# Kernel optimization log

Hardware: AMD Instinct MI355X
Metric: run time of the kernel (lower is better)

The kernel has to match this reference:

```python
import jax, jax.numpy as jnp
import numpy as np

L, D, H, B, T = 16, 256, 128, 32, 2048  # labels, input_dim, hidden (D//2), batch, seq_len


def setup_inputs() -> dict:
    key = jax.random.key(0)
    ks = jax.random.split(key, 6)
    inputs = jax.random.normal(ks[0], (B, T, D), dtype=jnp.float32)
    # variable lengths in [T//2, T], mask = 1 for valid positions
    lengths = jax.random.randint(ks[1], (B,), T // 2, T + 1)
    attention_mask = (jnp.arange(T)[None, :] < lengths[:, None]).astype(jnp.int32)
    s = 1.0 / np.sqrt(H)  # PyTorch GRU init range
    Wih = jax.random.uniform(ks[2], (L, 2, 3 * H, D), jnp.float32, -s, s)
    Whh = jax.random.uniform(ks[3], (L, 2, 3 * H, H), jnp.float32, -s, s)
    bih = jax.random.uniform(ks[4], (L, 2, 3 * H), jnp.float32, -s, s)
    bhh = jax.random.uniform(ks[5], (L, 2, 3 * H), jnp.float32, -s, s)
    label = jnp.arange(L, dtype=jnp.int64)
    return {"inputs": inputs, "attention_mask": attention_mask, "label": label,
            "Wih": Wih, "Whh": Whh, "bih": bih, "bhh": bhh}


def _gru_sweep(xs, mask, Wih, Whh, bih, bhh, reverse):
    """Run L independent GRUs over time with per-step validity masking.
    xs: [T,B,D], mask: [T,B] bool, Wih: [L,3H,D], Whh: [L,3H,H], bih/bhh: [L,3H].
    Returns final hidden [L,B,H]. Masked (padded) steps leave h unchanged, which
    for reverse=True reproduces packed-sequence backward-direction semantics
    (h0 carried untouched until t = len-1, then updated down to t = 0)."""
    h0 = jnp.zeros((Wih.shape[0], xs.shape[1], Whh.shape[-1]), xs.dtype)

    def step(h, inp):
        x_t, m_t = inp  # [B,D], [B]
        gi = jnp.einsum('bd,lgd->lbg', x_t, Wih) + bih[:, None, :]   # [L,B,3H]
        gh = jnp.einsum('lbh,lgh->lbg', h, Whh) + bhh[:, None, :]    # [L,B,3H]
        ir, iz, i_n = jnp.split(gi, 3, axis=-1)
        hr, hz, h_n = jnp.split(gh, 3, axis=-1)
        r = jax.nn.sigmoid(ir + hr)
        z = jax.nn.sigmoid(iz + hz)
        n = jnp.tanh(i_n + r * h_n)
        h_new = (1.0 - z) * n + z * h
        h = jnp.where(m_t[None, :, None], h_new, h)
        return h, None

    h_fin, _ = jax.lax.scan(step, h0, (xs, mask), reverse=reverse)
    return h_fin


def reference(inputs, attention_mask, label, Wih, Whh, bih, bhh):
    # select the GRUs for the given labels (train path iterates `label`)
    Wih_l, Whh_l = Wih[label], Whh[label]            # [L,2,3H,D], [L,2,3H,H]
    bih_l, bhh_l = bih[label], bhh[label]            # [L,2,3H]
    xs = jnp.transpose(inputs, (1, 0, 2))            # [T,B,D]
    mask = attention_mask.astype(bool).T             # [T,B]
    h_fwd = _gru_sweep(xs, mask, Wih_l[:, 0], Whh_l[:, 0], bih_l[:, 0], bhh_l[:, 0], reverse=False)
    h_bwd = _gru_sweep(xs, mask, Wih_l[:, 1], Whh_l[:, 1], bih_l[:, 1], bhh_l[:, 1], reverse=True)
    # torch.cat([h_n[-1], h_n[-2]]) = [backward_final, forward_final]
    out = jnp.concatenate([h_bwd, h_fwd], axis=-1)   # [L,B,2H]
    return jnp.transpose(out, (1, 0, 2))             # [B,L,2H] == [B,L,D]
```

## Files before the change

kernel.cpp:

```cpp
#include <hip/hip_runtime.h>


typedef unsigned short u16;
typedef unsigned int   u32;
using bf16x8 = __attribute__((ext_vector_type(8))) short;
using f32x4  = __attribute__((ext_vector_type(4))) float;

#define BLKW    1536
#define TSTRIDE 393216

#define KS_RZ (-1.4426950408889634f)
#define KS_N  (-2.8853900817779268f)

__device__ __forceinline__ u16 f2b(float f) {
  union { float f; u32 u; } v; v.f = f;
  u32 r = (v.u + 0x7fffu + ((v.u >> 16) & 1u)) >> 16;
  return (u16)r;
}
__device__ __forceinline__ u32 pack_bf16(float a, float b) {
#if __has_builtin(__builtin_amdgcn_cvt_pk_bf16_f32)
  auto pk = __builtin_amdgcn_cvt_pk_bf16_f32(a, b);
  union { decltype(pk) v; u32 u; } cv; cv.v = pk;
  return cv.u;
#else
  return (u32)f2b(a) | ((u32)f2b(b) << 16);
#endif
}
__device__ __forceinline__ float blo(u32 u) {
  union { u32 u; float f; } v; v.u = u << 16; return v.f;
}
__device__ __forceinline__ float bhi(u32 u) {
  union { u32 u; float f; } v; v.u = u & 0xffff0000u; return v.f;
}
__device__ __forceinline__ void lds16(u16* l, const u16* g) {
  __builtin_amdgcn_global_load_lds(
      (const __attribute__((address_space(1))) void*)g,
      (__attribute__((address_space(3))) void*)(unsigned long long)l,
      16, 0, 0);
}
__device__ __forceinline__ float sig2(float xs) {
  return __builtin_amdgcn_rcpf(1.f + __builtin_amdgcn_exp2f(xs));
}
__device__ __forceinline__ void softbarrier() {
  __builtin_amdgcn_sched_barrier(0);
  __builtin_amdgcn_s_waitcnt(0xC07F);
  __builtin_amdgcn_s_barrier();
  __builtin_amdgcn_sched_barrier(0);
}

__global__ void cvt_wih(const float* __restrict__ in, u16* __restrict__ o, int n) {
  int i = (blockIdx.x * 256 + threadIdx.x) * 4;
  if (i >= n) return;
  float s = (((i >> 15) % 3) == 2) ? KS_N : KS_RZ;
  float4 v = *(const float4*)(in + i);
  uint2 u; u.x = pack_bf16(v.x * s, v.y * s); u.y = pack_bf16(v.z * s, v.w * s);
  *(uint2*)(o + i) = u;
}
__global__ void cvt_whh(const float* __restrict__ in, u16* __restrict__ o, int n) {
  int i = (blockIdx.x * 256 + threadIdx.x) * 4;
  if (i >= n) return;
  float s = (((i >> 14) % 3) == 2) ? KS_N : KS_RZ;
  float4 v = *(const float4*)(in + i);
  uint2 u; u.x = pack_bf16(v.x * s, v.y * s); u.y = pack_bf16(v.z * s, v.w * s);
  *(uint2*)(o + i) = u;
}
__global__ void xpose(const float* __restrict__ x, u16* __restrict__ X) {
  int idx = blockIdx.x * 256 + threadIdx.x;
  int kc = idx & 63, tb = idx >> 6;
  int b = tb & 31, t = tb >> 5;
  float4 v = *(const float4*)(x + ((size_t)(b * 2048 + t) * 256 + kc * 4));
  uint2 u; u.x = pack_bf16(v.x, v.y); u.y = pack_bf16(v.z, v.w);
  *(uint2*)(X + ((size_t)tb * 256 + kc * 4)) = u;
}

__global__ __launch_bounds__(512, 1) void combo(
    const u16* __restrict__ X, const u16* __restrict__ Wib,
    const float* __restrict__ bih, const float* __restrict__ bhh,
    char* __restrict__ gw_f, char* __restrict__ gw_b, int tw_f, int tw_b, int n_gemm,
    const char* __restrict__ gr_f, const char* __restrict__ gr_b, int tr_f, int tr_b,
    const u16* __restrict__ Whb, const int* __restrict__ mask,
    float* __restrict__ hst, float* __restrict__ out,
    int Tc, int n_rec, int first, int last) {
  __shared__ __align__(16) char smem[49152];
  const int tid = threadIdx.x, lane = tid & 63;
  const int a = lane & 15, q = lane >> 4;

  if ((int)blockIdx.x >= n_rec) {
    const int g = blockIdx.x - n_rec;
    if (g >= n_gemm) return;
    const int mtiles = Tc >> 2;
    const int pair = g % 24;
    const int rest = g / 24;
    const int mb = rest % mtiles;
    const int dg = rest / mtiles;
    const int tbase = dg ? tw_b : tw_f;
    char* gi = dg ? gw_b : gw_f;

    const int w8 = tid >> 6, half = w8 >> 2, w4 = w8 & 3;
    const int mw = (w4 >> 1) * 64, nw = (w4 & 1) * 64;
    const int nti = pair * 2 + half;
    const int lidx = nti / 3, g3 = nti % 3, g0 = g3 * 128;

    u16* As = (u16*)smem;
    u16* Bs = (u16*)(smem + 16384 + half * 16384);
    const u16* Ag = X + (size_t)(tbase * 32 + mb * 128) * 256;
    const u16* Bg = Wib + (size_t)((lidx * 2 + dg) * 384 + g0) * 256;

    f32x4 acc[4][4];
    for (int i = 0; i < 4; ++i)
      for (int jj = 0; jj < 4; ++jj) acc[i][jj] = f32x4{0.f, 0.f, 0.f, 0.f};

    const int r8 = lane >> 3, kc = lane & 7;
    for (int kt = 0; kt < 4; ++kt) {
      for (int i = 0; i < 2; ++i) {
        int slot = w8 * 2 + i, row = slot * 8 + r8;
        lds16(&As[slot * 512 + lane * 8], Ag + (size_t)row * 256 + kt * 64 + kc * 8);
      }
      for (int i = 0; i < 4; ++i) {
        int slot = w4 * 4 + i, row = slot * 8 + r8;
        lds16(&Bs[slot * 512 + lane * 8], Bg + (size_t)row * 256 + kt * 64 + kc * 8);
      }
      __syncthreads();
      for (int ks = 0; ks < 2; ++ks) {
        bf16x8 Af[4], Bf[4];
        for (int mt = 0; mt < 4; ++mt)
          Af[mt] = *(const bf16x8*)&As[(mw + mt * 16 + a) * 64 + ks * 32 + q * 8];
        for (int nt = 0; nt < 4; ++nt)
          Bf[nt] = *(const bf16x8*)&Bs[(nw + nt * 16 + a) * 64 + ks * 32 + q * 8];
        for (int mt = 0; mt < 4; ++mt)
          for (int nt = 0; nt < 4; ++nt)
            acc[mt][nt] = __builtin_amdgcn_mfma_f32_16x16x32_bf16(
                Af[mt], Bf[nt], acc[mt][nt], 0, 0, 0);
      }
      __syncthreads();
    }
    for (int nt = 0; nt < 4; ++nt) {
      int gg = g0 + nw + nt * 16 + a;
      int gidx = (lidx * 2 + dg) * 384 + gg;
      float bias = (g3 == 2) ? KS_N * bih[gidx]
                             : KS_RZ * (bih[gidx] + bhh[gidx]);
      int wj = (nw + nt * 16) >> 4;
      for (int mt = 0; mt < 4; ++mt) {
        int rowbase = mb * 128 + mw + mt * 16;
        int t_loc = rowbase >> 5;
        int bh = (rowbase >> 4) & 1;
        uint2 uv;
        uv.x = pack_bf16(acc[mt][nt][0] + bias, acc[mt][nt][1] + bias);
        uv.y = pack_bf16(acc[mt][nt][2] + bias, acc[mt][nt][3] + bias);
        *(uint2*)(gi + (size_t)t_loc * TSTRIDE +
                  (size_t)((lidx * 2 + bh) * 8 + wj) * BLKW + g3 * 512 +
                  (q * 16 + a) * 8) = uv;
      }
    }
    return;
  }

  const int bid = blockIdx.x;
  const int bh = bid & 1, d = (bid >> 1) & 1, l = bid >> 2;
  const int w = tid >> 6;
  const int bbase = bh * 16;
  const int j = w * 16 + a;
  const int wofs = (l * 2 + d) * 384;

  u16* hb = (u16*)smem;
  int* lenS = (int*)(smem + 8704);

  bf16x8 Bf[3][4];
  for (int g3 = 0; g3 < 3; ++g3)
    for (int kf = 0; kf < 4; ++kf)
      Bf[g3][kf] = *(const bf16x8*)(Whb + (size_t)(wofs + g3 * 128 + j) * 128 + kf * 32 + q * 8);
  float bn = KS_N * bhh[wofs + 2 * 128 + j];
  f32x4 bc4 = f32x4{bn, bn, bn, bn};

  for (int rr = w; rr < 16; rr += 8) {
    int s = 0;
    const int* mp = mask + (size_t)(bbase + rr) * 2048;
    for (int t = lane; t < 2048; t += 64) s += mp[t];
    for (int off = 32; off; off >>= 1) s += __shfl_down(s, off);
    if (lane == 0) lenS[rr] = s;
  }

  float h[4];
  if (first) { h[0] = h[1] = h[2] = h[3] = 0.f; }
  else {
    for (int r = 0; r < 4; ++r)
      h[r] = hst[(size_t)((l * 2 + d) * 32 + bbase + q * 4 + r) * 128 + j];
  }
  {
    u32 k01 = pack_bf16(h[0], h[1]), k23 = pack_bf16(h[2], h[3]);
    u16* dst = &hb[(q * 4) * 136 + j];
    dst[0] = (u16)k01; dst[136] = (u16)(k01 >> 16);
    dst[272] = (u16)k23; dst[408] = (u16)(k23 >> 16);
  }
  __syncthreads();

  int len[4], mx = 0;
  for (int r = 0; r < 4; ++r) len[r] = lenS[q * 4 + r];
  for (int rr = 0; rr < 16; ++rr) mx = max(mx, lenS[rr]);

  const char* gi = d ? gr_b : gr_f;
  const int tb = d ? tr_b : tr_f;
  const size_t cbase = (size_t)((l * 2 + bh) * 8 + w) * BLKW + (q * 16 + a) * 8;

  int tl_lo, tl_hi;
  if (d == 0) { tl_lo = 0;
    int te = mx - tb;
    tl_hi = te <= 0 ? 0 : (te >= Tc ? Tc : ((te + 3) & ~3));
  } else { tl_hi = Tc;
    int ts = tb + Tc - mx;
    tl_lo = ts <= 0 ? 0 : (ts >= Tc ? Tc : (ts & ~3));
  }

  int p = 0;
  uint2 P[4][3];
  auto issue = [&](uint2 (&Pb)[3], int tl) {
    int tll = tl < Tc ? tl : Tc - 1;
    int t2 = d ? (Tc - 1 - tll) : tll;
    const char* bp = gi + (size_t)t2 * TSTRIDE + cbase;
    Pb[0] = *(const uint2*)(bp);
    Pb[1] = *(const uint2*)(bp + 512);
    Pb[2] = *(const uint2*)(bp + 1024);
  };
  issue(P[0], tl_lo); issue(P[1], tl_lo + 1);
  issue(P[2], tl_lo + 2); issue(P[3], tl_lo + 3);

  auto step = [&](int tl, uint2 (&Pb)[3]) {
    f32x4 Cr = f32x4{blo(Pb[0].x), bhi(Pb[0].x), blo(Pb[0].y), bhi(Pb[0].y)};
    f32x4 Cz = f32x4{blo(Pb[1].x), bhi(Pb[1].x), blo(Pb[1].y), bhi(Pb[1].y)};
    float nf[4] = { blo(Pb[2].x), bhi(Pb[2].x), blo(Pb[2].y), bhi(Pb[2].y) };
    issue(Pb, tl + 4);
    int t_loc = d ? (Tc - 1 - tl) : tl;
    int t_glob = tb + t_loc;

    bf16x8 Af[4];
    for (int kf = 0; kf < 4; ++kf)
      Af[kf] = *(const bf16x8*)&hb[p * 2176 + a * 136 + kf * 32 + q * 8];
    f32x4 a0 = __builtin_amdgcn_mfma_f32_16x16x32_bf16(Af[0], Bf[0][0], Cr, 0, 0, 0);
    f32x4 a1 = __builtin_amdgcn_mfma_f32_16x16x32_bf16(Af[0], Bf[1][0], Cz, 0, 0, 0);
    f32x4 a2 = __builtin_amdgcn_mfma_f32_16x16x32_bf16(Af[0], Bf[2][0], bc4, 0, 0, 0);
    for (int kf = 1; kf < 4; ++kf) {
      a0 = __builtin_amdgcn_mfma_f32_16x16x32_bf16(Af[kf], Bf[0][kf], a0, 0, 0, 0);
      a1 = __builtin_amdgcn_mfma_f32_16x16x32_bf16(Af[kf], Bf[1][kf], a1, 0, 0, 0);
      a2 = __builtin_amdgcn_mfma_f32_16x16x32_bf16(Af[kf], Bf[2][kf], a2, 0, 0, 0);
    }
    for (int r = 0; r < 4; ++r) {
      float rg = sig2(a0[r]);
      float zg = sig2(a1[r]);
      float ng = fmaf(2.f, sig2(fmaf(rg, a2[r], nf[r])), -1.f);
      float hv = fmaf(zg, h[r] - ng, ng);
      h[r] = (t_glob < len[r]) ? hv : h[r];
    }
    u32 k01 = pack_bf16(h[0], h[1]), k23 = pack_bf16(h[2], h[3]);
    u16* dst = &hb[(p ^ 1) * 2176 + (q * 4) * 136 + j];
    dst[0] = (u16)k01; dst[136] = (u16)(k01 >> 16);
    dst[272] = (u16)k23; dst[408] = (u16)(k23 >> 16);
    softbarrier();
    p ^= 1;
  };

  for (int tl = tl_lo; tl < tl_hi; tl += 4) {
    step(tl, P[0]);
    step(tl + 1, P[1]);
    step(tl + 2, P[2]);
    step(tl + 3, P[3]);
  }

  if (last) {
    for (int r = 0; r < 4; ++r)
      out[(size_t)((bbase + q * 4 + r) * 16 + l) * 256 + (d ? j : 128 + j)] = h[r];
  } else {
    for (int r = 0; r < 4; ++r)
      hst[(size_t)((l * 2 + d) * 32 + bbase + q * 4 + r) * 128 + j] = h[r];
  }
}

extern "C" void kernel_launch(void* const* d_in, const int* in_sizes, int n_in,
                              void* d_out, int out_size, void* d_ws, size_t ws_size,
                              hipStream_t stream) {
  const float* x    = (const float*)d_in[0];
  const int*   mask = (const int*)d_in[1];
  const float* Wih  = (const float*)d_in[3];
  const float* Whh  = (const float*)d_in[4];
  const float* bih  = (const float*)d_in[5];
  const float* bhh  = (const float*)d_in[6];
  float* out = (float*)d_out;

  char* ws = (char*)d_ws;
  size_t off = 0;
  auto alloc = [&](size_t bytes) -> void* {
    void* p = ws + off; off += (bytes + 255) & ~(size_t)255; return p;
  };
  u16*  Wib = (u16*)alloc(3145728ull * 2);
  u16*  Whb = (u16*)alloc(1572864ull * 2);
  u16*  X   = (u16*)alloc(16777216ull * 2);
  float* hst = (float*)alloc(131072ull * 4);
  size_t fixed = off;

  int Tc = 2048;
  while (Tc > 8 && fixed + 4ull * Tc * TSTRIDE > ws_size) Tc >>= 1;
  char* gi[2][2];
  for (int pp = 0; pp < 2; ++pp)
    for (int dd = 0; dd < 2; ++dd)
      gi[pp][dd] = (char*)alloc((size_t)Tc * TSTRIDE);
  int Nc = 2048 / Tc;
  int NG = 24 * (Tc / 4) * 2;

  cvt_wih<<<3145728 / 4 / 256, 256, 0, stream>>>(Wih, Wib, 3145728);
  cvt_whh<<<1572864 / 4 / 256, 256, 0, stream>>>(Whh, Whb, 1572864);
  xpose<<<16384, 256, 0, stream>>>(x, X);

  combo<<<NG, 512, 0, stream>>>(X, Wib, bih, bhh,
                                gi[0][0], gi[0][1], 0, (Nc - 1) * Tc, NG,
                                gi[0][0], gi[0][1], 0, 0,
                                Whb, mask, hst, out, Tc, 0, 0, 0);

  for (int c = 0; c < Nc; ++c) {
    int par = c & 1, parn = par ^ 1;
    int hasg = (c + 1 < Nc);
    int ng = hasg ? NG : 0;
    combo<<<64 + ng, 512, 0, stream>>>(X, Wib, bih, bhh,
        gi[parn][0], gi[parn][1], (c + 1) * Tc, (Nc - 2 - c) * Tc, ng,
        gi[par][0], gi[par][1], c * Tc, (Nc - 1 - c) * Tc,
        Whb, mask, hst, out, Tc, 64, c == 0, c == Nc - 1);
  }
}
```

Baseline: 1.506 ms.

## Split recurrent blocks to 8 batch rows each, doubling recurrence block count

Each recurrent block now owns 8 batch rows instead of 16, so 128 recurrent blocks run instead of 64 and each thread carries 2 hidden values instead of 4. The precomputed input-gate buffer is relaid out to a 768-byte per-warp stride with 4-byte per-lane loads to match. Launch bounds move to 2 blocks per CU. The MFMA still computes 16 rows with half of them padding, so the per-step latency chain stays about the same while the elementwise work per thread halves. The intent is to spread the serial recurrence across more CUs and shorten each step, at the cost of wasted MFMA rows and twice the Whh register loads across blocks.

```diff
diff --git a/kernel.cpp b/kernel.cpp
--- a/kernel.cpp
+++ b/kernel.cpp
@@ -6,8 +6,8 @@
 using bf16x8 = __attribute__((ext_vector_type(8))) short;
 using f32x4  = __attribute__((ext_vector_type(4))) float;
 
-#define BLKW    1536
 #define TSTRIDE 393216
+#define BLKW    768
 
 #define KS_RZ (-1.4426950408889634f)
 #define KS_N  (-2.8853900817779268f)
@@ -73,7 +73,7 @@
   *(uint2*)(X + ((size_t)tb * 256 + kc * 4)) = u;
 }
 
-__global__ __launch_bounds__(512, 1) void combo(
+__global__ __launch_bounds__(512, 2) void combo(
     const u16* __restrict__ X, const u16* __restrict__ Wib,
     const float* __restrict__ bih, const float* __restrict__ bhh,
     char* __restrict__ gw_f, char* __restrict__ gw_b, int tw_f, int tw_b, int n_gemm,
@@ -139,26 +139,28 @@
       int gidx = (lidx * 2 + dg) * 384 + gg;
       float bias = (g3 == 2) ? KS_N * bih[gidx]
                              : KS_RZ * (bih[gidx] + bhh[gidx]);
-      int wj = (nw + nt * 16) >> 4;
+      int wj = ((nw + nt * 16) >> 4);
       for (int mt = 0; mt < 4; ++mt) {
         int rowbase = mb * 128 + mw + mt * 16;
         int t_loc = rowbase >> 5;
-        int bh = (rowbase >> 4) & 1;
-        uint2 uv;
-        uv.x = pack_bf16(acc[mt][nt][0] + bias, acc[mt][nt][1] + bias);
-        uv.y = pack_bf16(acc[mt][nt][2] + bias, acc[mt][nt][3] + bias);
-        *(uint2*)(gi + (size_t)t_loc * TSTRIDE +
-                  (size_t)((lidx * 2 + bh) * 8 + wj) * BLKW + g3 * 512 +
-                  (q * 16 + a) * 8) = uv;
+        int b0 = (rowbase & 31) + q * 4;
+        int bq0 = b0 >> 3, q0 = (b0 >> 1) & 3;
+        int bq1 = (b0 + 2) >> 3, q1 = ((b0 + 2) >> 1) & 3;
+        char* p0 = gi + (size_t)t_loc * TSTRIDE +
+                   (size_t)((lidx * 4 + bq0) * 8 + wj) * BLKW + g3 * 256 + (q0 * 16 + a) * 4;
+        char* p1 = gi + (size_t)t_loc * TSTRIDE +
+                   (size_t)((lidx * 4 + bq1) * 8 + wj) * BLKW + g3 * 256 + (q1 * 16 + a) * 4;
+        *(u32*)p0 = pack_bf16(acc[mt][nt][0] + bias, acc[mt][nt][1] + bias);
+        *(u32*)p1 = pack_bf16(acc[mt][nt][2] + bias, acc[mt][nt][3] + bias);
       }
     }
     return;
   }
 
   const int bid = blockIdx.x;
-  const int bh = bid & 1, d = (bid >> 1) & 1, l = bid >> 2;
+  const int bq = bid & 3, d = (bid >> 2) & 1, l = bid >> 3;
   const int w = tid >> 6;
-  const int bbase = bh * 16;
+  const int bbase = bq * 8;
   const int j = w * 16 + a;
   const int wofs = (l * 2 + d) * 384;
 
@@ -172,35 +174,34 @@
   float bn = KS_N * bhh[wofs + 2 * 128 + j];
   f32x4 bc4 = f32x4{bn, bn, bn, bn};
 
-  for (int rr = w; rr < 16; rr += 8) {
+  if (w < 8) {
     int s = 0;
-    const int* mp = mask + (size_t)(bbase + rr) * 2048;
+    const int* mp = mask + (size_t)(bbase + w) * 2048;
     for (int t = lane; t < 2048; t += 64) s += mp[t];
     for (int off = 32; off; off >>= 1) s += __shfl_down(s, off);
-    if (lane == 0) lenS[rr] = s;
-  }
-
-  float h[4];
-  if (first) { h[0] = h[1] = h[2] = h[3] = 0.f; }
+    if (lane == 0) lenS[w] = s;
+  }
+
+  float h0, h1;
+  if (first) { h0 = h1 = 0.f; }
   else {
-    for (int r = 0; r < 4; ++r)
-      h[r] = hst[(size_t)((l * 2 + d) * 32 + bbase + q * 4 + r) * 128 + j];
+    h0 = hst[(size_t)((l * 2 + d) * 32 + bbase + q * 2 + 0) * 128 + j];
+    h1 = hst[(size_t)((l * 2 + d) * 32 + bbase + q * 2 + 1) * 128 + j];
   }
   {
-    u32 k01 = pack_bf16(h[0], h[1]), k23 = pack_bf16(h[2], h[3]);
+    u32 k = pack_bf16(h0, h1);
     u16* dst = &hb[(q * 4) * 136 + j];
-    dst[0] = (u16)k01; dst[136] = (u16)(k01 >> 16);
-    dst[272] = (u16)k23; dst[408] = (u16)(k23 >> 16);
+    dst[0] = (u16)k; dst[136] = (u16)(k >> 16);
   }
   __syncthreads();
 
-  int len[4], mx = 0;
-  for (int r = 0; r < 4; ++r) len[r] = lenS[q * 4 + r];
-  for (int rr = 0; rr < 16; ++rr) mx = max(mx, lenS[rr]);
+  int len0 = lenS[q * 2 + 0], len1 = lenS[q * 2 + 1];
+  int mx = 0;
+  for (int rr = 0; rr < 8; ++rr) mx = max(mx, lenS[rr]);
 
   const char* gi = d ? gr_b : gr_f;
   const int tb = d ? tr_b : tr_f;
-  const size_t cbase = (size_t)((l * 2 + bh) * 8 + w) * BLKW + (q * 16 + a) * 8;
+  const char* gbase = gi + (size_t)((l * 4 + bq) * 8 + w) * BLKW + lane * 4;
 
   int tl_lo, tl_hi;
   if (d == 0) { tl_lo = 0;
@@ -212,22 +213,22 @@
   }
 
   int p = 0;
-  uint2 P[4][3];
-  auto issue = [&](uint2 (&Pb)[3], int tl) {
+  uint3 P[4];
+  auto issue = [&](uint3& Pb, int tl) {
     int tll = tl < Tc ? tl : Tc - 1;
     int t2 = d ? (Tc - 1 - tll) : tll;
-    const char* bp = gi + (size_t)t2 * TSTRIDE + cbase;
-    Pb[0] = *(const uint2*)(bp);
-    Pb[1] = *(const uint2*)(bp + 512);
-    Pb[2] = *(const uint2*)(bp + 1024);
+    const char* bp = gbase + (size_t)t2 * TSTRIDE;
+    Pb.x = *(const u32*)(bp);
+    Pb.y = *(const u32*)(bp + 256);
+    Pb.z = *(const u32*)(bp + 512);
   };
   issue(P[0], tl_lo); issue(P[1], tl_lo + 1);
   issue(P[2], tl_lo + 2); issue(P[3], tl_lo + 3);
 
-  auto step = [&](int tl, uint2 (&Pb)[3]) {
-    f32x4 Cr = f32x4{blo(Pb[0].x), bhi(Pb[0].x), blo(Pb[0].y), bhi(Pb[0].y)};
-    f32x4 Cz = f32x4{blo(Pb[1].x), bhi(Pb[1].x), blo(Pb[1].y), bhi(Pb[1].y)};
-    float nf[4] = { blo(Pb[2].x), bhi(Pb[2].x), blo(Pb[2].y), bhi(Pb[2].y) };
+  auto step = [&](int tl, uint3& Pb) {
+    f32x4 Cr = f32x4{blo(Pb.x), bhi(Pb.x), 0.f, 0.f};
+    f32x4 Cz = f32x4{blo(Pb.y), bhi(Pb.y), 0.f, 0.f};
+    float nf0 = blo(Pb.z), nf1 = bhi(Pb.z);
     issue(Pb, tl + 4);
     int t_loc = d ? (Tc - 1 - tl) : tl;
     int t_glob = tb + t_loc;
@@ -243,17 +244,23 @@
       a1 = __builtin_amdgcn_mfma_f32_16x16x32_bf16(Af[kf], Bf[1][kf], a1, 0, 0, 0);
       a2 = __builtin_amdgcn_mfma_f32_16x16x32_bf16(Af[kf], Bf[2][kf], a2, 0, 0, 0);
     }
-    for (int r = 0; r < 4; ++r) {
-      float rg = sig2(a0[r]);
-      float zg = sig2(a1[r]);
-      float ng = fmaf(2.f, sig2(fmaf(rg, a2[r], nf[r])), -1.f);
-      float hv = fmaf(zg, h[r] - ng, ng);
-      h[r] = (t_glob < len[r]) ? hv : h[r];
-    }
-    u32 k01 = pack_bf16(h[0], h[1]), k23 = pack_bf16(h[2], h[3]);
+    {
+      float rg = sig2(a0[0]);
+      float zg = sig2(a1[0]);
+      float ng = fmaf(2.f, sig2(fmaf(rg, a2[0], nf0)), -1.f);
+      float hv = fmaf(zg, h0 - ng, ng);
+      h0 = (t_glob < len0) ? hv : h0;
+    }
+    {
+      float rg = sig2(a0[1]);
+      float zg = sig2(a1[1]);
+      float ng = fmaf(2.f, sig2(fmaf(rg, a2[1], nf1)), -1.f);
+      float hv = fmaf(zg, h1 - ng, ng);
+      h1 = (t_glob < len1) ? hv : h1;
+    }
+    u32 k = pack_bf16(h0, h1);
     u16* dst = &hb[(p ^ 1) * 2176 + (q * 4) * 136 + j];
-    dst[0] = (u16)k01; dst[136] = (u16)(k01 >> 16);
-    dst[272] = (u16)k23; dst[408] = (u16)(k23 >> 16);
+    dst[0] = (u16)k; dst[136] = (u16)(k >> 16);
     softbarrier();
     p ^= 1;
   };
@@ -266,11 +273,11 @@
   }
 
   if (last) {
-    for (int r = 0; r < 4; ++r)
-      out[(size_t)((bbase + q * 4 + r) * 16 + l) * 256 + (d ? j : 128 + j)] = h[r];
+    out[(size_t)((bbase + q * 2 + 0) * 16 + l) * 256 + (d ? j : 128 + j)] = h0;
+    out[(size_t)((bbase + q * 2 + 1) * 16 + l) * 256 + (d ? j : 128 + j)] = h1;
   } else {
-    for (int r = 0; r < 4; ++r)
-      hst[(size_t)((l * 2 + d) * 32 + bbase + q * 4 + r) * 128 + j] = h[r];
+    hst[(size_t)((l * 2 + d) * 32 + bbase + q * 2 + 0) * 128 + j] = h0;
+    hst[(size_t)((l * 2 + d) * 32 + bbase + q * 2 + 1) * 128 + j] = h1;
   }
 }
 
@@ -318,9 +325,9 @@
     int par = c & 1, parn = par ^ 1;
     int hasg = (c + 1 < Nc);
     int ng = hasg ? NG : 0;
-    combo<<<64 + ng, 512, 0, stream>>>(X, Wib, bih, bhh,
+    combo<<<128 + ng, 512, 0, stream>>>(X, Wib, bih, bhh,
         gi[parn][0], gi[parn][1], (c + 1) * Tc, (Nc - 2 - c) * Tc, ng,
         gi[par][0], gi[par][1], c * Tc, (Nc - 1 - c) * Tc,
-        Whb, mask, hst, out, Tc, 64, c == 0, c == Nc - 1);
-  }
-}
+        Whb, mask, hst, out, Tc, 128, c == 0, c == Nc - 1);
+  }
+}
```

Result: slower. 1.562 ms (+3.7%).

## Run GRU recurrence on four waves each owning two hidden column tiles

Applied to the files above, without the earlier changes.

The recurrent step is redistributed so only four of the eight waves compute, each handling two 16-column tiles of the hidden state with six MFMA chains instead of three. The gate-precompute layout and the LDS hidden buffer layout change to match, with 16-byte loads of precomputed gates and a new transposed hb indexing. The prefetch depth drops from four steps to two. The other four waves only participate in the soft barriers. This aims to cut per-step synchronisation cost and LDS traffic among fewer waves, at the cost of more serial work per wave and shallower prefetch.

```diff
diff --git a/kernel.cpp b/kernel.cpp
--- a/kernel.cpp
+++ b/kernel.cpp
@@ -6,8 +6,8 @@
 using bf16x8 = __attribute__((ext_vector_type(8))) short;
 using f32x4  = __attribute__((ext_vector_type(4))) float;
 
-#define BLKW    1536
 #define TSTRIDE 393216
+#define BLKW    3072
 
 #define KS_RZ (-1.4426950408889634f)
 #define KS_N  (-2.8853900817779268f)
@@ -135,11 +135,11 @@
       __syncthreads();
     }
     for (int nt = 0; nt < 4; ++nt) {
-      int gg = g0 + nw + nt * 16 + a;
-      int gidx = (lidx * 2 + dg) * 384 + gg;
+      int j = nw + nt * 16 + a;
+      int gidx = (lidx * 2 + dg) * 384 + g0 + j;
       float bias = (g3 == 2) ? KS_N * bih[gidx]
                              : KS_RZ * (bih[gidx] + bhh[gidx]);
-      int wj = (nw + nt * 16) >> 4;
+      int wj = j >> 5, ct = (j >> 4) & 1;
       for (int mt = 0; mt < 4; ++mt) {
         int rowbase = mb * 128 + mw + mt * 16;
         int t_loc = rowbase >> 5;
@@ -148,8 +148,8 @@
         uv.x = pack_bf16(acc[mt][nt][0] + bias, acc[mt][nt][1] + bias);
         uv.y = pack_bf16(acc[mt][nt][2] + bias, acc[mt][nt][3] + bias);
         *(uint2*)(gi + (size_t)t_loc * TSTRIDE +
-                  (size_t)((lidx * 2 + bh) * 8 + wj) * BLKW + g3 * 512 +
-                  (q * 16 + a) * 8) = uv;
+                  (size_t)((lidx * 2 + bh) * 4 + wj) * BLKW + g3 * 1024 +
+                  (q * 16 + a) * 16 + ct * 8) = uv;
       }
     }
     return;
@@ -159,118 +159,153 @@
   const int bh = bid & 1, d = (bid >> 1) & 1, l = bid >> 2;
   const int w = tid >> 6;
   const int bbase = bh * 16;
-  const int j = w * 16 + a;
   const int wofs = (l * 2 + d) * 384;
+  const int jc0 = w * 32 + a, jc1 = jc0 + 16;
 
   u16* hb = (u16*)smem;
-  int* lenS = (int*)(smem + 8704);
-
-  bf16x8 Bf[3][4];
-  for (int g3 = 0; g3 < 3; ++g3)
-    for (int kf = 0; kf < 4; ++kf)
-      Bf[g3][kf] = *(const bf16x8*)(Whb + (size_t)(wofs + g3 * 128 + j) * 128 + kf * 32 + q * 8);
-  float bn = KS_N * bhh[wofs + 2 * 128 + j];
-  f32x4 bc4 = f32x4{bn, bn, bn, bn};
-
-  for (int rr = w; rr < 16; rr += 8) {
+  int* lenS = (int*)(smem + 8192);
+
+  {
     int s = 0;
-    const int* mp = mask + (size_t)(bbase + rr) * 2048;
+    const int* mp = mask + (size_t)(bbase + w) * 2048;
     for (int t = lane; t < 2048; t += 64) s += mp[t];
     for (int off = 32; off; off >>= 1) s += __shfl_down(s, off);
-    if (lane == 0) lenS[rr] = s;
-  }
-
-  float h[4];
-  if (first) { h[0] = h[1] = h[2] = h[3] = 0.f; }
-  else {
-    for (int r = 0; r < 4; ++r)
-      h[r] = hst[(size_t)((l * 2 + d) * 32 + bbase + q * 4 + r) * 128 + j];
-  }
-  {
-    u32 k01 = pack_bf16(h[0], h[1]), k23 = pack_bf16(h[2], h[3]);
-    u16* dst = &hb[(q * 4) * 136 + j];
-    dst[0] = (u16)k01; dst[136] = (u16)(k01 >> 16);
-    dst[272] = (u16)k23; dst[408] = (u16)(k23 >> 16);
+    if (lane == 0) lenS[w] = s;
+    s = 0;
+    mp = mask + (size_t)(bbase + w + 8) * 2048;
+    for (int t = lane; t < 2048; t += 64) s += mp[t];
+    for (int off = 32; off; off >>= 1) s += __shfl_down(s, off);
+    if (lane == 0) lenS[w + 8] = s;
+  }
+
+  float h[2][4];
+  if (w < 4) {
+    for (int ct = 0; ct < 2; ++ct) {
+      int jc = ct ? jc1 : jc0;
+      for (int r = 0; r < 4; ++r)
+        h[ct][r] = first ? 0.f
+            : hst[(size_t)((l * 2 + d) * 32 + bbase + q * 4 + r) * 128 + jc];
+      u32 k01 = pack_bf16(h[ct][0], h[ct][1]);
+      u32 k23 = pack_bf16(h[ct][2], h[ct][3]);
+      u16* dst = &hb[(w * 4 + ct * 2 + (a >> 3)) * 128 + (q * 4) * 8 + (a & 7)];
+      dst[0] = (u16)k01; dst[8] = (u16)(k01 >> 16);
+      dst[16] = (u16)k23; dst[24] = (u16)(k23 >> 16);
+    }
   }
   __syncthreads();
 
-  int len[4], mx = 0;
+  int len[4];
   for (int r = 0; r < 4; ++r) len[r] = lenS[q * 4 + r];
+  int mx = 0;
   for (int rr = 0; rr < 16; ++rr) mx = max(mx, lenS[rr]);
 
   const char* gi = d ? gr_b : gr_f;
   const int tb = d ? tr_b : tr_f;
-  const size_t cbase = (size_t)((l * 2 + bh) * 8 + w) * BLKW + (q * 16 + a) * 8;
 
   int tl_lo, tl_hi;
   if (d == 0) { tl_lo = 0;
     int te = mx - tb;
-    tl_hi = te <= 0 ? 0 : (te >= Tc ? Tc : ((te + 3) & ~3));
+    tl_hi = te <= 0 ? 0 : (te >= Tc ? Tc : ((te + 1) & ~1));
   } else { tl_hi = Tc;
     int ts = tb + Tc - mx;
-    tl_lo = ts <= 0 ? 0 : (ts >= Tc ? Tc : (ts & ~3));
-  }
-
+    tl_lo = ts <= 0 ? 0 : (ts >= Tc ? Tc : (ts & ~1));
+  }
+
+  if (w >= 4) {
+    for (int i = tl_lo; i < tl_hi; ++i) softbarrier();
+    return;
+  }
+
+  bf16x8 Bf[3][2][4];
+  for (int g3 = 0; g3 < 3; ++g3)
+    for (int ct = 0; ct < 2; ++ct)
+      for (int kf = 0; kf < 4; ++kf)
+        Bf[g3][ct][kf] = *(const bf16x8*)(
+            Whb + (size_t)(wofs + g3 * 128 + (ct ? jc1 : jc0)) * 128 + kf * 32 + q * 8);
+  float bn0 = KS_N * bhh[wofs + 256 + jc0];
+  float bn1 = KS_N * bhh[wofs + 256 + jc1];
+  f32x4 bc0 = f32x4{bn0, bn0, bn0, bn0};
+  f32x4 bc1 = f32x4{bn1, bn1, bn1, bn1};
+
+  const char* gbase = gi + (size_t)(((l * 2 + bh) * 4 + w)) * BLKW + lane * 16;
+
+  struct GI { uint4 r, z, n; };
   int p = 0;
-  uint2 P[4][3];
-  auto issue = [&](uint2 (&Pb)[3], int tl) {
+  GI P[2];
+  auto issue = [&](GI& Pb, int tl) {
     int tll = tl < Tc ? tl : Tc - 1;
     int t2 = d ? (Tc - 1 - tll) : tll;
-    const char* bp = gi + (size_t)t2 * TSTRIDE + cbase;
-    Pb[0] = *(const uint2*)(bp);
-    Pb[1] = *(const uint2*)(bp + 512);
-    Pb[2] = *(const uint2*)(bp + 1024);
+    const char* bp = gbase + (size_t)t2 * TSTRIDE;
+    Pb.r = *(const uint4*)(bp);
+    Pb.z = *(const uint4*)(bp + 1024);
+    Pb.n = *(const uint4*)(bp + 2048);
   };
   issue(P[0], tl_lo); issue(P[1], tl_lo + 1);
-  issue(P[2], tl_lo + 2); issue(P[3], tl_lo + 3);
-
-  auto step = [&](int tl, uint2 (&Pb)[3]) {
-    f32x4 Cr = f32x4{blo(Pb[0].x), bhi(Pb[0].x), blo(Pb[0].y), bhi(Pb[0].y)};
-    f32x4 Cz = f32x4{blo(Pb[1].x), bhi(Pb[1].x), blo(Pb[1].y), bhi(Pb[1].y)};
-    float nf[4] = { blo(Pb[2].x), bhi(Pb[2].x), blo(Pb[2].y), bhi(Pb[2].y) };
-    issue(Pb, tl + 4);
-    int t_loc = d ? (Tc - 1 - tl) : tl;
-    int t_glob = tb + t_loc;
+
+  auto step = [&](int tl, GI& Pb) {
+    f32x4 Cr0 = f32x4{blo(Pb.r.x), bhi(Pb.r.x), blo(Pb.r.y), bhi(Pb.r.y)};
+    f32x4 Cr1 = f32x4{blo(Pb.r.z), bhi(Pb.r.z), blo(Pb.r.w), bhi(Pb.r.w)};
+    f32x4 Cz0 = f32x4{blo(Pb.z.x), bhi(Pb.z.x), blo(Pb.z.y), bhi(Pb.z.y)};
+    f32x4 Cz1 = f32x4{blo(Pb.z.z), bhi(Pb.z.z), blo(Pb.z.w), bhi(Pb.z.w)};
+    float nf0[4] = { blo(Pb.n.x), bhi(Pb.n.x), blo(Pb.n.y), bhi(Pb.n.y) };
+    float nf1[4] = { blo(Pb.n.z), bhi(Pb.n.z), blo(Pb.n.w), bhi(Pb.n.w) };
+    issue(Pb, tl + 2);
+    int t_glob = tb + (d ? (Tc - 1 - tl) : tl);
 
     bf16x8 Af[4];
     for (int kf = 0; kf < 4; ++kf)
-      Af[kf] = *(const bf16x8*)&hb[p * 2176 + a * 136 + kf * 32 + q * 8];
-    f32x4 a0 = __builtin_amdgcn_mfma_f32_16x16x32_bf16(Af[0], Bf[0][0], Cr, 0, 0, 0);
-    f32x4 a1 = __builtin_amdgcn_mfma_f32_16x16x32_bf16(Af[0], Bf[1][0], Cz, 0, 0, 0);
-    f32x4 a2 = __builtin_amdgcn_mfma_f32_16x16x32_bf16(Af[0], Bf[2][0], bc4, 0, 0, 0);
-    for (int kf = 1; kf < 4; ++kf) {
-      a0 = __builtin_amdgcn_mfma_f32_16x16x32_bf16(Af[kf], Bf[0][kf], a0, 0, 0, 0);
-      a1 = __builtin_amdgcn_mfma_f32_16x16x32_bf16(Af[kf], Bf[1][kf], a1, 0, 0, 0);
-      a2 = __builtin_amdgcn_mfma_f32_16x16x32_bf16(Af[kf], Bf[2][kf], a2, 0, 0, 0);
+      Af[kf] = *(const bf16x8*)&hb[p * 2048 + (kf * 4 + q) * 128 + a * 8];
+    f32x4 r0 = Cr0, r1 = Cr1, z0 = Cz0, z1 = Cz1, n0 = bc0, n1 = bc1;
+    for (int kf = 0; kf < 4; ++kf) {
+      r0 = __builtin_amdgcn_mfma_f32_16x16x32_bf16(Af[kf], Bf[0][0][kf], r0, 0, 0, 0);
+      r1 = __builtin_amdgcn_mfma_f32_16x16x32_bf16(Af[kf], Bf[0][1][kf], r1, 0, 0, 0);
+      z0 = __builtin_amdgcn_mfma_f32_16x16x32_bf16(Af[kf], Bf[1][0][kf], z0, 0, 0, 0);
+      z1 = __builtin_amdgcn_mfma_f32_16x16x32_bf16(Af[kf], Bf[1][1][kf], z1, 0, 0, 0);
+      n0 = __builtin_amdgcn_mfma_f32_16x16x32_bf16(Af[kf], Bf[2][0][kf], n0, 0, 0, 0);
+      n1 = __builtin_amdgcn_mfma_f32_16x16x32_bf16(Af[kf], Bf[2][1][kf], n1, 0, 0, 0);
     }
     for (int r = 0; r < 4; ++r) {
-      float rg = sig2(a0[r]);
-      float zg = sig2(a1[r]);
-      float ng = fmaf(2.f, sig2(fmaf(rg, a2[r], nf[r])), -1.f);
-      float hv = fmaf(zg, h[r] - ng, ng);
-      h[r] = (t_glob < len[r]) ? hv : h[r];
-    }
-    u32 k01 = pack_bf16(h[0], h[1]), k23 = pack_bf16(h[2], h[3]);
-    u16* dst = &hb[(p ^ 1) * 2176 + (q * 4) * 136 + j];
-    dst[0] = (u16)k01; dst[136] = (u16)(k01 >> 16);
-    dst[272] = (u16)k23; dst[408] = (u16)(k23 >> 16);
+      {
+        float rg = sig2(r0[r]);
+        float zg = sig2(z0[r]);
+        float ng = fmaf(2.f, sig2(fmaf(rg, n0[r], nf0[r])), -1.f);
+        float hv = fmaf(zg, h[0][r] - ng, ng);
+        h[0][r] = (t_glob < len[r]) ? hv : h[0][r];
+      }
+      {
+        float rg = sig2(r1[r]);
+        float zg = sig2(z1[r]);
+        float ng = fmaf(2.f, sig2(fmaf(rg, n1[r], nf1[r])), -1.f);
+        float hv = fmaf(zg, h[1][r] - ng, ng);
+        h[1][r] = (t_glob < len[r]) ? hv : h[1][r];
+      }
+    }
+    for (int ct = 0; ct < 2; ++ct) {
+      u32 k01 = pack_bf16(h[ct][0], h[ct][1]);
+      u32 k23 = pack_bf16(h[ct][2], h[ct][3]);
+      u16* dst = &hb[(p ^ 1) * 2048 +
+                     (w * 4 + ct * 2 + (a >> 3)) * 128 + (q * 4) * 8 + (a & 7)];
+      dst[0] = (u16)k01; dst[8] = (u16)(k01 >> 16);
+      dst[16] = (u16)k23; dst[24] = (u16)(k23 >> 16);
+    }
     softbarrier();
     p ^= 1;
   };
 
-  for (int tl = tl_lo; tl < tl_hi; tl += 4) {
+  for (int tl = tl_lo; tl < tl_hi; tl += 2) {
     step(tl, P[0]);
     step(tl + 1, P[1]);
-    step(tl + 2, P[2]);
-    step(tl + 3, P[3]);
-  }
-
-  if (last) {
-    for (int r = 0; r < 4; ++r)
-      out[(size_t)((bbase + q * 4 + r) * 16 + l) * 256 + (d ? j : 128 + j)] = h[r];
-  } else {
-    for (int r = 0; r < 4; ++r)
-      hst[(size_t)((l * 2 + d) * 32 + bbase + q * 4 + r) * 128 + j] = h[r];
+  }
+
+  for (int ct = 0; ct < 2; ++ct) {
+    int jc = ct ? jc1 : jc0;
+    if (last) {
+      for (int r = 0; r < 4; ++r)
+        out[(size_t)((bbase + q * 4 + r) * 16 + l) * 256 + (d ? jc : 128 + jc)] = h[ct][r];
+    } else {
+      for (int r = 0; r < 4; ++r)
+        hst[(size_t)((l * 2 + d) * 32 + bbase + q * 4 + r) * 128 + jc] = h[ct][r];
+    }
   }
 }
 
```

Measured after the change: 1.606 ms. +6.6%, slower.
